# Performance work log

Hardware: AMD Instinct MI355X
Metric: run time of the kernel (lower is better)

Reference implementation:

```python
import jax, jax.numpy as jnp
import numpy as np

B, T, D = 256, 128, 1024
H = 128          # lstm_hidden
CF = 128         # conv_filters
K = 9            # num_labels
CE_W = 0.2
EPS = 1e-5


def conv1d(x, w, b, pad):
    # x: (B, C, T), w: (O, I, k)
    y = jax.lax.conv_general_dilated(x, w, (1,), [(pad, pad)],
                                     dimension_numbers=('NCH', 'OIH', 'NCH'))
    return y + b[None, :, None]


def batchnorm(x, g, beta):
    # training-mode BN over (N, W) per channel, biased variance (torch default)
    m = x.mean(axis=(0, 2), keepdims=True)
    v = x.var(axis=(0, 2), keepdims=True)
    return (x - m) * jax.lax.rsqrt(v + EPS) * g[None, :, None] + beta[None, :, None]


def lstm_dir(x, Wih, Whh, bih, bhh, reverse):
    # x: (B, T, D_in). PyTorch gate order: i, f, g, o.
    xg = jnp.einsum('btd,gd->btg', x, Wih) + bih + bhh  # (B, T, 4H)
    h0 = jnp.zeros((x.shape[0], Whh.shape[1]), x.dtype)
    c0 = jnp.zeros_like(h0)

    def step(carry, g_t):
        h, c = carry
        gates = g_t + h @ Whh.T
        i, f, g, o = jnp.split(gates, 4, axis=-1)
        c = jax.nn.sigmoid(f) * c + jax.nn.sigmoid(i) * jnp.tanh(g)
        h = jax.nn.sigmoid(o) * jnp.tanh(c)
        return (h, c), h

    _, hs = jax.lax.scan(step, (h0, c0), jnp.swapaxes(xg, 0, 1), reverse=reverse)
    return jnp.swapaxes(hs, 0, 1)  # (B, T, H)


def crf_log_partition(em, mask, start, trans, end):
    # em: (B, T, K), mask: (B, T) bool (mask[:,0] assumed True)
    score = start[None, :] + em[:, 0]  # (B, K)

    def step(score, inp):
        em_t, m_t = inp  # (B, K), (B,)
        nxt = jax.nn.logsumexp(score[:, :, None] + trans[None] + em_t[:, None, :], axis=1)
        return jnp.where(m_t[:, None], nxt, score), None

    score, _ = jax.lax.scan(step, score,
                            (jnp.swapaxes(em[:, 1:], 0, 1), jnp.swapaxes(mask[:, 1:], 0, 1)))
    return jax.nn.logsumexp(score + end[None, :], axis=1)  # (B,)


def crf_numerator(em, tags, mask, start, trans, end):
    mf = mask.astype(em.dtype)
    em_sc = jnp.take_along_axis(em, tags[..., None], axis=-1)[..., 0]  # (B, T)
    tr_sc = trans[tags[:, :-1], tags[:, 1:]]                           # (B, T-1)
    seq_ends = mask.astype(jnp.int32).sum(axis=1) - 1
    last_tags = jnp.take_along_axis(tags, seq_ends[:, None], axis=1)[:, 0]
    return (start[tags[:, 0]] + em_sc[:, 0]
            + ((tr_sc + em_sc[:, 1:]) * mf[:, 1:]).sum(axis=1)
            + end[last_tags])


def setup_inputs() -> dict:
    key = jax.random.key(0)
    ks = jax.random.split(key, 32)
    s = 0.05
    inp = {
        'embeddings': jax.random.normal(ks[0], (B, T, D), jnp.float32),
        'attention_mask': jnp.ones((B, T), jnp.int32),
        'labels': jax.random.randint(ks[1], (B, T), 0, K).astype(jnp.int64),
        'conv5_w': jax.random.normal(ks[2], (CF, D, 5)) * s,
        'conv5_b': jnp.zeros((CF,)),
        'bn1_g': jnp.ones((CF,)),
        'bn1_b': jnp.zeros((CF,)),
        'Wih_f': jax.random.normal(ks[3], (4 * H, CF)) * s,
        'Whh_f': jax.random.normal(ks[4], (4 * H, H)) * s,
        'bih_f': jnp.zeros((4 * H,)),
        'bhh_f': jnp.zeros((4 * H,)),
        'Wih_b': jax.random.normal(ks[5], (4 * H, CF)) * s,
        'Whh_b': jax.random.normal(ks[6], (4 * H, H)) * s,
        'bih_b': jnp.zeros((4 * H,)),
        'bhh_b': jnp.zeros((4 * H,)),
        'conv7_w': jax.random.normal(ks[7], (CF, 2 * H, 7)) * s,
        'conv7_b': jnp.zeros((CF,)),
        'conv9_w': jax.random.normal(ks[8], (CF, 2 * H, 9)) * s,
        'conv9_b': jnp.zeros((CF,)),
        'bn2_g': jnp.ones((2 * CF,)),
        'bn2_b': jnp.zeros((2 * CF,)),
        'cls_w': jax.random.normal(ks[9], (K, 2 * CF)) * s,
        'cls_b': jnp.zeros((K,)),
        'crf_start': jax.random.normal(ks[10], (K,)) * 0.1,
        'crf_trans': jax.random.normal(ks[11], (K, K)) * 0.1,
        'crf_end': jax.random.normal(ks[12], (K,)) * 0.1,
        'class_weights': jax.random.uniform(ks[13], (K,)) + 0.5,
    }
    return inp


def reference(embeddings, attention_mask, labels, conv5_w, conv5_b, bn1_g, bn1_b,
              Wih_f, Whh_f, bih_f, bhh_f, Wih_b, Whh_b, bih_b, bhh_b,
              conv7_w, conv7_b, conv9_w, conv9_b, bn2_g, bn2_b, cls_w, cls_b,
              crf_start, crf_trans, crf_end, class_weights):
    x = embeddings.astype(jnp.float32)
    xt = jnp.swapaxes(x, 1, 2)  # (B, D, T)
    xc = jax.nn.gelu(batchnorm(conv1d(xt, conv5_w, conv5_b, 2), bn1_g, bn1_b),
                     approximate=False)
    xl = jnp.swapaxes(xc, 1, 2)  # (B, T, CF)
    hf = lstm_dir(xl, Wih_f, Whh_f, bih_f, bhh_f, reverse=False)
    hb = lstm_dir(xl, Wih_b, Whh_b, bih_b, bhh_b, reverse=True)
    lstm_out = jnp.swapaxes(jnp.concatenate([hf, hb], axis=-1), 1, 2)  # (B, 2H, T)
    c7 = conv1d(lstm_out, conv7_w, conv7_b, 3)
    c9 = conv1d(lstm_out, conv9_w, conv9_b, 4)
    feat = jax.nn.gelu(batchnorm(jnp.concatenate([c7, c9], axis=1), bn2_g, bn2_b),
                       approximate=False)
    feat = jnp.swapaxes(feat, 1, 2)  # (B, T, 2CF); dropout p=0 -> identity
    logits = jnp.einsum('btf,kf->btk', feat, cls_w) + cls_b  # (B, T, K)

    mask = (attention_mask != 0) & (labels != -100)
    mod_labels = jnp.where(labels == -100, 0, labels).astype(jnp.int32)

    num = crf_numerator(logits, mod_labels, mask, crf_start, crf_trans, crf_end)
    logZ = crf_log_partition(logits, mask, crf_start, crf_trans, crf_end)
    crf_loss = -(num - logZ).mean()

    logp = jax.nn.log_softmax(logits, axis=-1).reshape(-1, K)
    y = labels.reshape(-1)
    valid = y != -100
    yi = jnp.where(valid, y, 0).astype(jnp.int32)
    nll = -jnp.take_along_axis(logp, yi[:, None], axis=1)[:, 0]
    w = jnp.where(valid, class_weights[yi], 0.0)
    ce_loss = (w * nll).sum() / w.sum()

    return (1.0 - CE_W) * crf_loss + CE_W * ce_loss
```

## Files before the change

kernel.cpp:

```cpp
#include <hip/hip_runtime.h>
#include <hip/hip_bf16.h>
#include <math.h>

#define BB 256
#define TT 128
#define DD 1024
#define CFF 128
#define HH 128
#define G4 512
#define NK 9

typedef __attribute__((ext_vector_type(8))) short bf16x8;
typedef __attribute__((ext_vector_type(4))) float f32x4;

__device__ __forceinline__ float bf_lo(unsigned u){ union{unsigned u; float f;} v; v.u = u << 16; return v.f; }
__device__ __forceinline__ float bf_hi(unsigned u){ union{unsigned u; float f;} v; v.u = u & 0xffff0000u; return v.f; }
__device__ __forceinline__ unsigned f2bf(float x){
    union{float f; unsigned u;} v; v.f = x;
    unsigned r = v.u + 0x7fffu + ((v.u >> 16) & 1u);
    return r >> 16;
}
__device__ __forceinline__ float fsig_fast(float x){
    return __builtin_amdgcn_rcpf(1.0f + __builtin_amdgcn_exp2f(-1.44269504f * x));
}
__device__ __forceinline__ float ftanh_fast(float x){
    return 1.0f - 2.0f * __builtin_amdgcn_rcpf(1.0f + __builtin_amdgcn_exp2f(2.88539008f * x));
}
__device__ __forceinline__ float gelu_exact(float x){
    return 0.5f*x*(1.0f + erff(x*0.70710678118654752440f));
}

__global__ __launch_bounds__(256) void prep_convw_kernel(
    const float* __restrict__ w, ushort* __restrict__ Wk, int CIN, int KS, int total)
{
    int i = blockIdx.x*256 + threadIdx.x;
    if (i >= total) return;
    int k = i % KS;
    int d = (i / KS) % CIN;
    int f = i / (KS * CIN);
    Wk[((size_t)(k*128 + f))*CIN + d] = (ushort)f2bf(w[i]);
}

__global__ __launch_bounds__(256) void prep_xg_kernel(
    const float* __restrict__ Wf, const float* __restrict__ Wb,
    const float* __restrict__ bif, const float* __restrict__ bhf,
    const float* __restrict__ bib, const float* __restrict__ bhb,
    ushort* __restrict__ Wxg, float* __restrict__ bias_xg)
{
    int i = blockIdx.x*256 + threadIdx.x;
    if (i < 65536) Wxg[i] = (ushort)f2bf(Wf[i]);
    else if (i < 131072) Wxg[i] = (ushort)f2bf(Wb[i - 65536]);
    else {
        int j = i - 131072;
        if (j < 512) bias_xg[j] = bif[j] + bhf[j];
        else if (j < 1024) bias_xg[j] = bib[j-512] + bhb[j-512];
    }
}

template<int CIN, int KS, int KSE_MAX, int SPLIT, bool IN_F32, bool OUT_BF16, bool XGT = false>
__global__ __launch_bounds__(256, 1) void conv_mfma_kernel(
    const void* __restrict__ in_v,
    const ushort* __restrict__ Wk_g,
    const float* __restrict__ bias_g,
    void* __restrict__ outA_v, void* __restrict__ outB_v,
    int OS, int co)
{
    constexpr int PAD = KS / 2;
    constexpr int ROWS = 128 + 2 * PAD;
    constexpr int NSTEP = (SPLIT == 1) ? (CIN / 64) : (CIN / 32);
    constexpr int ATOT = IN_F32 ? ROWS * 8 : ROWS * 4;
    constexpr int BTOT = KSE_MAX * 128 * 4;
    constexpr int AIT = (ATOT + 255) / 256;
    constexpr int BIT = (BTOT + 255) / 256;

    __shared__ ushort A_lds[ROWS * 32];
    __shared__ ushort B_lds[KSE_MAX * 128 * 32];

    const int tid = threadIdx.x;
    const int b   = blockIdx.x;
    const int by  = blockIdx.y;
    const int z   = blockIdx.z;
    const int dbase = (SPLIT == 1) ? z * (CIN / 2) : 0;
    const int k0    = (SPLIT == 2) ? z * KSE_MAX : 0;
    const int kse   = (SPLIT == 2) ? ((z == 0) ? KSE_MAX : (KS - KSE_MAX)) : KS;
    const ushort* __restrict__ Wk = Wk_g + (size_t)by * (size_t)(128 * CIN);
    const float* __restrict__ bias = bias_g + by * 128;

    float4 aRf[AIT];
    int4   aRb[AIT];
    int4   bR[BIT];

    auto stage_load = [&](int s) {
        const int d0 = dbase + s * 32;
        if constexpr (IN_F32) {
            const float* __restrict__ inp = (const float*)in_v;
#pragma unroll
            for (int it = 0; it < AIT; ++it) {
                int i = tid + it * 256;
                float4 v = make_float4(0.f, 0.f, 0.f, 0.f);
                if (i < ATOT) {
                    int r = i >> 3, c = i & 7;
                    int t = r - PAD;
                    if (t >= 0 && t < TT)
                        v = *reinterpret_cast<const float4*>(&inp[((size_t)b * TT + t) * CIN + d0 + c * 4]);
                }
                aRf[it] = v;
            }
        } else {
            const ushort* __restrict__ inp = (const ushort*)in_v;
#pragma unroll
            for (int it = 0; it < AIT; ++it) {
                int i = tid + it * 256;
                int4 v = make_int4(0, 0, 0, 0);
                if (i < ATOT) {
                    int r = i >> 2, c = i & 3;
                    int t = r - PAD;
                    if (t >= 0 && t < TT)
                        v = *reinterpret_cast<const int4*>(&inp[((size_t)b * TT + t) * CIN + d0 + c * 8]);
                }
                aRb[it] = v;
            }
        }
#pragma unroll
        for (int it = 0; it < BIT; ++it) {
            int i = tid + it * 256;
            int kk = i >> 9;
            int rem = i & 511;
            int f = rem >> 2, c = rem & 3;
            int4 v = make_int4(0, 0, 0, 0);
            if (kk < kse)
                v = *reinterpret_cast<const int4*>(&Wk[((size_t)((k0 + kk) * 128 + f)) * CIN + d0 + c * 8]);
            bR[it] = v;
        }
    };

    auto stage_write = [&]() {
        if constexpr (IN_F32) {
#pragma unroll
            for (int it = 0; it < AIT; ++it) {
                int i = tid + it * 256;
                if (i < ATOT) {
                    int r = i >> 3, c = i & 7;
                    float4 v = aRf[it];
                    ushort4 h;
                    h.x = (ushort)f2bf(v.x); h.y = (ushort)f2bf(v.y);
                    h.z = (ushort)f2bf(v.z); h.w = (ushort)f2bf(v.w);
                    int slot = (c >> 1) ^ (r & 3);
                    *reinterpret_cast<ushort4*>(&A_lds[r * 32 + slot * 8 + (c & 1) * 4]) = h;
                }
            }
        } else {
#pragma unroll
            for (int it = 0; it < AIT; ++it) {
                int i = tid + it * 256;
                if (i < ATOT) {
                    int r = i >> 2, c = i & 3;
                    int slot = c ^ (r & 3);
                    *reinterpret_cast<int4*>(&A_lds[r * 32 + slot * 8]) = aRb[it];
                }
            }
        }
#pragma unroll
        for (int it = 0; it < BIT; ++it) {
            int i = tid + it * 256;
            int kk = i >> 9;
            int rem = i & 511;
            int f = rem >> 2, c = rem & 3;
            int slot = c ^ (f & 3);
            *reinterpret_cast<int4*>(&B_lds[(kk * 128 + f) * 32 + slot * 8]) = bR[it];
        }
    };

    const int lane = tid & 63;
    const int wave = tid >> 6;
    const int lr = lane & 15;
    const int lk = lane >> 4;
    const int wm = wave >> 1;
    const int wn = wave & 1;

    f32x4 acc[4][4];
#pragma unroll
    for (int m = 0; m < 4; ++m)
#pragma unroll
        for (int n = 0; n < 4; ++n)
            acc[m][n] = (f32x4){0.f, 0.f, 0.f, 0.f};

    stage_load(0);
    stage_write();
    asm volatile("s_waitcnt lgkmcnt(0)" ::: "memory");
    __builtin_amdgcn_s_barrier();
    __builtin_amdgcn_sched_barrier(0);

    for (int s = 0; s < NSTEP; ++s) {
        if (s + 1 < NSTEP) stage_load(s + 1);
#pragma unroll
        for (int kk = 0; kk < KSE_MAX; ++kk) {
            bf16x8 af[4], bfr[4];
#pragma unroll
            for (int m = 0; m < 4; ++m) {
                int R = wm * 64 + m * 16 + lr + k0 + kk;
                if (kk >= kse) R = 0;
                af[m] = *reinterpret_cast<const bf16x8*>(&A_lds[R * 32 + ((lk ^ (R & 3)) * 8)]);
            }
#pragma unroll
            for (int n = 0; n < 4; ++n) {
                int Rb = kk * 128 + wn * 64 + n * 16 + lr;
                bfr[n] = *reinterpret_cast<const bf16x8*>(&B_lds[Rb * 32 + ((lk ^ (lr & 3)) * 8)]);
            }
#pragma unroll
            for (int m = 0; m < 4; ++m)
#pragma unroll
                for (int n = 0; n < 4; ++n)
                    acc[m][n] = __builtin_amdgcn_mfma_f32_16x16x32_bf16(af[m], bfr[n], acc[m][n], 0, 0, 0);
        }
        if (s + 1 < NSTEP) {
            asm volatile("s_waitcnt lgkmcnt(0)" ::: "memory");
            __builtin_amdgcn_s_barrier();
            __builtin_amdgcn_sched_barrier(0);
            stage_write();
            asm volatile("s_waitcnt lgkmcnt(0)" ::: "memory");
            __builtin_amdgcn_s_barrier();
            __builtin_amdgcn_sched_barrier(0);
        }
    }

    const bool addb = (SPLIT == 0) || (z == 0);
    void* out_v = (SPLIT != 0 && z == 1) ? outB_v : outA_v;
    float bv[4];
#pragma unroll
    for (int n = 0; n < 4; ++n) bv[n] = addb ? bias[wn * 64 + n * 16 + lr] : 0.f;
#pragma unroll
    for (int m = 0; m < 4; ++m) {
#pragma unroll
        for (int n = 0; n < 4; ++n) {
            int f = wn * 64 + n * 16 + lr;
#pragma unroll
            for (int q = 0; q < 4; ++q) {
                int trow = wm * 64 + m * 16 + lk * 4 + q;
                float val = acc[m][n][q] + bv[n];
                size_t idx;
                if constexpr (XGT) {
                    int dirg = by >> 2;
                    int g = by & 3;
                    idx = (size_t)dirg * 16777216u + (size_t)trow * 131072u
                        + (size_t)b * 512u + (size_t)(g * 128 + f);
                } else {
                    idx = ((size_t)b * TT + trow) * (size_t)OS + co + f;
                }
                if constexpr (OUT_BF16)
                    ((ushort*)out_v)[idx] = (ushort)f2bf(val);
                else
                    ((float*)out_v)[idx] = val;
            }
        }
    }
}

__global__ __launch_bounds__(256) void bn_stats_kernel(
    const float* __restrict__ y, const float* __restrict__ y2, int C, int rows_per_blk,
    float* __restrict__ sum, float* __restrict__ sqsum)
{
    int tpc = 256 / C;
    int c = threadIdx.x & (C - 1);
    int sub = threadIdx.x / C;
    size_t r0 = (size_t)blockIdx.x * rows_per_blk;
    float s = 0.f, s2 = 0.f;
    for (int r = sub; r < rows_per_blk; r += tpc) {
        size_t i = (r0 + r)*C + c;
        float v = y[i] + y2[i];
        s += v; s2 += v*v;
    }
    __shared__ float ls[256], ls2[256];
    ls[threadIdx.x] = s; ls2[threadIdx.x] = s2;
    __syncthreads();
    if (sub == 0) {
        for (int k = 1; k < tpc; ++k) { s += ls[c + k*C]; s2 += ls2[c + k*C]; }
        atomicAdd(&sum[c], s);
        atomicAdd(&sqsum[c], s2);
    }
}

__global__ __launch_bounds__(256) void bn_gelu_bf16_kernel(
    const float* __restrict__ y, const float* __restrict__ y2,
    const float* __restrict__ sum, const float* __restrict__ sqsum,
    const float* __restrict__ g, const float* __restrict__ beta,
    ushort* __restrict__ out, float inv_n)
{
    size_t i = (size_t)blockIdx.x*256 + threadIdx.x;
    int c = (int)(i & 127);
    float m = sum[c] * inv_n;
    float var = fmaxf(sqsum[c]*inv_n - m*m, 0.f);
    float xv = (y[i] + y2[i] - m) * rsqrtf(var + 1e-5f) * g[c] + beta[c];
    out[i] = (ushort)f2bf(gelu_exact(xv));
}

__global__ __launch_bounds__(512, 1) void lstm_mfma_kernel(
    const ushort* __restrict__ xg2,
    const float* __restrict__ Whhf, const float* __restrict__ Whhb,
    ushort* __restrict__ hfb)
{
    const int tid = threadIdx.x;
    const int lane = tid & 63;
    const int w = tid >> 6;
    const int jc = lane & 15;
    const int kq = lane >> 4;
    const int dir = blockIdx.x >> 4;
    const int b0 = (blockIdx.x & 15) << 4;
    const float* __restrict__ Whh = dir ? Whhb : Whhf;

    bf16x8 Wf[4][4];
#pragma unroll
    for (int g = 0; g < 4; ++g) {
        const float* wr = &Whh[(size_t)((g << 7) + (w << 4) + jc) * HH + (kq << 3)];
#pragma unroll
        for (int s = 0; s < 4; ++s) {
            float4 v0 = *reinterpret_cast<const float4*>(wr + (s << 5));
            float4 v1 = *reinterpret_cast<const float4*>(wr + (s << 5) + 4);
            union { bf16x8 v; ushort u[8]; } pk;
            pk.u[0] = (ushort)f2bf(v0.x); pk.u[1] = (ushort)f2bf(v0.y);
            pk.u[2] = (ushort)f2bf(v0.z); pk.u[3] = (ushort)f2bf(v0.w);
            pk.u[4] = (ushort)f2bf(v1.x); pk.u[5] = (ushort)f2bf(v1.y);
            pk.u[6] = (ushort)f2bf(v1.z); pk.u[7] = (ushort)f2bf(v1.w);
            Wf[g][s] = pk.v;
        }
    }

    __shared__ ushort h_lds[2][16 * 136];
    for (int i = tid; i < 16 * 136; i += 512) h_lds[0][i] = 0;
    f32x4 creg = (f32x4){0.f, 0.f, 0.f, 0.f};

    const int col0 = (w << 4) + (kq << 2);
    const int hrd = jc * 136 + (kq << 3);

    const ptrdiff_t dstep = dir ? -131072 : 131072;
    const int tt0 = dir ? (TT - 1) : 0;
    const ushort* pA = xg2 + (size_t)dir * 16777216u + (size_t)(b0 + jc) * 512u
                     + (size_t)col0 + (size_t)tt0 * 131072u;
    const ushort* pB = pA + dstep;

    uint2 xA[4], xB[4];
#pragma unroll
    for (int g = 0; g < 4; ++g) {
        xA[g] = *reinterpret_cast<const uint2*>(pA + (g << 7));
        xB[g] = *reinterpret_cast<const uint2*>(pB + (g << 7));
    }
    pA += 2 * dstep;
    pB += 2 * dstep;

    ushort* hp = hfb + (size_t)(b0 + jc) * (TT * 256) + (size_t)tt0 * 256
               + (dir << 7) + col0;
    const ptrdiff_t hstep = dir ? -256 : 256;

    __syncthreads();

    int cur = 0;

    auto step = [&](uint2 (&xr)[4], const ushort*& pp) {
        f32x4 acc[4];
#pragma unroll
        for (int g = 0; g < 4; ++g) {
            acc[g][0] = bf_lo(xr[g].x);
            acc[g][1] = bf_hi(xr[g].x);
            acc[g][2] = bf_lo(xr[g].y);
            acc[g][3] = bf_hi(xr[g].y);
        }
#pragma unroll
        for (int g = 0; g < 4; ++g)
            xr[g] = *reinterpret_cast<const uint2*>(pp + (g << 7));
        pp += 2 * dstep;
        bf16x8 Hf[4];
#pragma unroll
        for (int s = 0; s < 4; ++s)
            Hf[s] = *reinterpret_cast<const bf16x8*>(&h_lds[cur][hrd + (s << 5)]);
#pragma unroll
        for (int s = 0; s < 4; ++s)
#pragma unroll
            for (int g = 0; g < 4; ++g)
                acc[g] = __builtin_amdgcn_mfma_f32_16x16x32_bf16(Wf[g][s], Hf[s], acc[g], 0, 0, 0);
        float hv[4];
#pragma unroll
        for (int r = 0; r < 4; ++r) {
            float iv = fsig_fast(acc[0][r]);
            float fv = fsig_fast(acc[1][r]);
            float gv = ftanh_fast(acc[2][r]);
            float ov = fsig_fast(acc[3][r]);
            float c = fv * creg[r] + iv * gv;
            creg[r] = c;
            hv[r] = ov * ftanh_fast(c);
        }
        uint2 hb;
        asm("v_cvt_pk_bf16_f32 %0, %1, %2" : "=v"(hb.x) : "v"(hv[0]), "v"(hv[1]));
        asm("v_cvt_pk_bf16_f32 %0, %1, %2" : "=v"(hb.y) : "v"(hv[2]), "v"(hv[3]));
        const int nxt = cur ^ 1;
        *reinterpret_cast<uint2*>(&h_lds[nxt][jc * 136 + col0]) = hb;
        asm volatile("s_waitcnt lgkmcnt(0)" ::: "memory");
        __builtin_amdgcn_s_barrier();
        __builtin_amdgcn_sched_barrier(0);
        *reinterpret_cast<uint2*>(hp) = hb;
        hp += hstep;
        cur = nxt;
    };

    for (int t = 0; t < TT; t += 2) {
        step(xA, pA);
        step(xB, pB);
    }
}

__global__ __launch_bounds__(256) void logits_bn_kernel(
    const float* __restrict__ a, const float* __restrict__ bpart,
    const float* __restrict__ sum, const float* __restrict__ sqsum,
    const float* __restrict__ g, const float* __restrict__ beta,
    const float* __restrict__ cw, const float* __restrict__ cb,
    float* __restrict__ lg, float inv_n)
{
    __shared__ float wls[NK*256];
    __shared__ float sc_lds[256], sh_lds[256];
    for (int i = threadIdx.x; i < NK*256; i += 256) wls[i] = cw[i];
    {
        int c = threadIdx.x;
        float m = sum[c] * inv_n;
        float var = fmaxf(sqsum[c]*inv_n - m*m, 0.f);
        float rs = rsqrtf(var + 1e-5f);
        float s = rs * g[c];
        sc_lds[c] = s;
        sh_lds[c] = beta[c] - m * s;
    }
    __syncthreads();
    size_t row = (size_t)blockIdx.x*256 + threadIdx.x;
    const float* ar = &a[row*256];
    const float* br = &bpart[row*256];
    float acc[NK];
#pragma unroll
    for (int k = 0; k < NK; ++k) acc[k] = 0.f;
    for (int c = 0; c < 256; c += 4) {
        float4 av = *reinterpret_cast<const float4*>(&ar[c]);
        float4 bv = *reinterpret_cast<const float4*>(&br[c]);
        float vv[4] = {av.x + bv.x, av.y + bv.y, av.z + bv.z, av.w + bv.w};
#pragma unroll
        for (int j = 0; j < 4; ++j) {
            float xv = vv[j] * sc_lds[c + j] + sh_lds[c + j];
            float f = gelu_exact(xv);
#pragma unroll
            for (int k = 0; k < NK; ++k)
                acc[k] += f * wls[k*256 + c + j];
        }
    }
#pragma unroll
    for (int k = 0; k < NK; ++k) lg[row*NK + k] = acc[k] + cb[k];
}

__global__ __launch_bounds__(256) void ce_kernel(
    const float* __restrict__ lg, const int* __restrict__ labels,
    const float* __restrict__ cw, float* __restrict__ acc2)
{
    size_t i = (size_t)blockIdx.x*256 + threadIdx.x;
    const float* l = &lg[i*NK];
    float mx = -1e30f;
#pragma unroll
    for (int k = 0; k < NK; ++k) mx = fmaxf(mx, l[k]);
    float se = 0.f;
#pragma unroll
    for (int k = 0; k < NK; ++k) se += expf(l[k] - mx);
    float lz = mx + logf(se);
    int y = labels[i];
    bool valid = (y != -100);
    int yi = valid ? y : 0;
    float nll = lz - l[yi];
    float wv = valid ? cw[yi] : 0.f;
    __shared__ float s1[256], s2[256];
    s1[threadIdx.x] = wv*nll;
    s2[threadIdx.x] = wv;
    __syncthreads();
    for (int s = 128; s > 0; s >>= 1) {
        if (threadIdx.x < s) { s1[threadIdx.x] += s1[threadIdx.x + s]; s2[threadIdx.x] += s2[threadIdx.x + s]; }
        __syncthreads();
    }
    if (threadIdx.x == 0) { atomicAdd(&acc2[0], s1[0]); atomicAdd(&acc2[1], s2[0]); }
}

__global__ __launch_bounds__(64) void crf_kernel(
    const float* __restrict__ lg, const int* __restrict__ att,
    const int* __restrict__ labels, const float* __restrict__ startv,
    const float* __restrict__ trans, const float* __restrict__ endv,
    float* __restrict__ numo, float* __restrict__ logzo)
{
    int b = blockIdx.x;
    int lane = threadIdx.x;
    int lane_c = (lane < NK) ? lane : 0;
    const float* em = &lg[(size_t)b*TT*NK];
    float tr[NK];
#pragma unroll
    for (int i = 0; i < NK; ++i) tr[i] = trans[i*NK + lane_c];
    float score = startv[lane_c] + em[lane_c];

    for (int t = 1; t < TT; ++t) {
        int lt = labels[b*TT + t];
        bool m = (att[b*TT + t] != 0) && (lt != -100);
        float vals[NK];
#pragma unroll
        for (int i = 0; i < NK; ++i)
            vals[i] = __shfl(score, i, 64) + tr[i];
        if (m) {
            float mx = vals[0];
#pragma unroll
            for (int i = 1; i < NK; ++i) mx = fmaxf(mx, vals[i]);
            float sm = 0.f;
#pragma unroll
            for (int i = 0; i < NK; ++i) sm += expf(vals[i] - mx);
            score = mx + logf(sm) + em[t*NK + lane_c];
        }
    }
    float fin = (lane < NK) ? (score + endv[lane_c]) : -1e30f;
    float mx = -1e30f;
#pragma unroll
    for (int i = 0; i < NK; ++i) mx = fmaxf(mx, __shfl(fin, i, 64));
    float sm = 0.f;
#pragma unroll
    for (int i = 0; i < NK; ++i) sm += expf(__shfl(fin, i, 64) - mx);
    if (lane == 0) logzo[b] = mx + logf(sm);

    if (lane == 0) {
        int l0 = labels[b*TT];
        int tag0 = (l0 == -100) ? 0 : l0;
        bool m0 = (att[b*TT] != 0) && (l0 != -100);
        float num = startv[tag0] + em[tag0];
        int prev = tag0;
        int cnt = m0 ? 1 : 0;
        for (int t = 1; t < TT; ++t) {
            int lt = labels[b*TT + t];
            bool m = (att[b*TT + t] != 0) && (lt != -100);
            int tag = (lt == -100) ? 0 : lt;
            if (m) { num += trans[prev*NK + tag] + em[t*NK + tag]; cnt++; }
            prev = tag;
        }
        int le = cnt - 1; if (le < 0) le = 0; if (le >= TT) le = TT - 1;
        int ll = labels[b*TT + le];
        int ltag = (ll == -100) ? 0 : ll;
        num += endv[ltag];
        numo[b] = num;
    }
}

__global__ __launch_bounds__(256) void finalize_kernel(
    const float* __restrict__ numo, const float* __restrict__ logzo,
    const float* __restrict__ acc2, float* __restrict__ out)
{
    __shared__ float red[256];
    int tid = threadIdx.x;
    red[tid] = numo[tid] - logzo[tid];
    __syncthreads();
    for (int s = 128; s > 0; s >>= 1) {
        if (tid < s) red[tid] += red[tid + s];
        __syncthreads();
    }
    if (tid == 0) {
        float crf = -(red[0] / (float)BB);
        float ce = acc2[0] / acc2[1];
        out[0] = 0.8f*crf + 0.2f*ce;
    }
}

extern "C" void kernel_launch(void* const* d_in, const int* in_sizes, int n_in,
                              void* d_out, int out_size, void* d_ws, size_t ws_size,
                              hipStream_t stream)
{
    const float* emb   = (const float*)d_in[0];
    const int*   att   = (const int*)  d_in[1];
    const int*   lab   = (const int*)  d_in[2];
    const float* c5w   = (const float*)d_in[3];
    const float* c5b   = (const float*)d_in[4];
    const float* bn1g  = (const float*)d_in[5];
    const float* bn1b  = (const float*)d_in[6];
    const float* Wihf  = (const float*)d_in[7];
    const float* Whhf  = (const float*)d_in[8];
    const float* bihf  = (const float*)d_in[9];
    const float* bhhf  = (const float*)d_in[10];
    const float* Wihb  = (const float*)d_in[11];
    const float* Whhb  = (const float*)d_in[12];
    const float* bihb  = (const float*)d_in[13];
    const float* bhhb  = (const float*)d_in[14];
    const float* c7w   = (const float*)d_in[15];
    const float* c7b   = (const float*)d_in[16];
    const float* c9w   = (const float*)d_in[17];
    const float* c9b   = (const float*)d_in[18];
    const float* bn2g  = (const float*)d_in[19];
    const float* bn2b  = (const float*)d_in[20];
    const float* clsw  = (const float*)d_in[21];
    const float* clsb  = (const float*)d_in[22];
    const float* cstart= (const float*)d_in[23];
    const float* ctrans= (const float*)d_in[24];
    const float* cend  = (const float*)d_in[25];
    const float* cwts  = (const float*)d_in[26];
    (void)in_sizes; (void)n_in; (void)out_size; (void)ws_size;

    char* wsb = (char*)d_ws;
    size_t off = 0;
    auto alloc = [&](size_t bytes) { void* p = wsb + off; off += (bytes + 255) & ~(size_t)255; return p; };
    float*  y1      = (float*) alloc((size_t)4194304*4);
    ushort* xg      = (ushort*)alloc((size_t)2*16777216*2);
    ushort* hfb     = (ushort*)alloc((size_t)8388608*2);
    ushort* y1h     = (ushort*)alloc((size_t)4194304*2);
    float*  lg      = (float*) alloc((size_t)294912*4);
    ushort* Wk5     = (ushort*)alloc((size_t)655360*2);
    ushort* Wk7     = (ushort*)alloc((size_t)229376*2);
    ushort* Wk9     = (ushort*)alloc((size_t)294912*2);
    ushort* Wxg     = (ushort*)alloc((size_t)131072*2);
    float*  bias_xg = (float*) alloc((size_t)1024*4);
    float*  stats   = (float*) alloc((size_t)2048*4);
    float* y1b  = (float*)xg;
    float* c79a = (float*)xg;
    float* c79b = (float*)(xg + 16777216);
    float* bn1s = stats;
    float* bn1q = stats + 128;
    float* bn2s = stats + 256;
    float* bn2q = stats + 512;
    float* acc2 = stats + 768;
    float* numo = stats + 770;
    float* logzo = numo + 256;

    hipMemsetAsync(stats, 0, 770*sizeof(float), stream);

    prep_convw_kernel<<<2560, 256, 0, stream>>>(c5w, Wk5, 1024, 5, 655360);
    prep_convw_kernel<<<896,  256, 0, stream>>>(c7w, Wk7, 256, 7, 229376);
    prep_convw_kernel<<<1152, 256, 0, stream>>>(c9w, Wk9, 256, 9, 294912);
    prep_xg_kernel<<<516, 256, 0, stream>>>(Wihf, Wihb, bihf, bhhf, bihb, bhhb, Wxg, bias_xg);

    conv_mfma_kernel<1024,5,5,1,true,false><<<dim3(256,1,2), 256, 0, stream>>>(emb, Wk5, c5b, y1, y1b, 128, 0);
    bn_stats_kernel<<<256, 256, 0, stream>>>(y1, y1b, 128, 128, bn1s, bn1q);
    bn_gelu_bf16_kernel<<<16384, 256, 0, stream>>>(y1, y1b, bn1s, bn1q, bn1g, bn1b, y1h, 1.0f/32768.f);

    conv_mfma_kernel<128,1,1,0,false,true,true><<<dim3(256,8,1), 256, 0, stream>>>(y1h, Wxg, bias_xg, xg, nullptr, 512, 0);
    lstm_mfma_kernel<<<32, 512, 0, stream>>>(xg, Whhf, Whhb, hfb);

    conv_mfma_kernel<256,7,4,2,false,false><<<dim3(256,1,2), 256, 0, stream>>>(hfb, Wk7, c7b, c79a, c79b, 256, 0);
    conv_mfma_kernel<256,9,5,2,false,false><<<dim3(256,1,2), 256, 0, stream>>>(hfb, Wk9, c9b, c79a, c79b, 256, 128);
    bn_stats_kernel<<<256, 256, 0, stream>>>(c79a, c79b, 256, 128, bn2s, bn2q);

    logits_bn_kernel<<<128, 256, 0, stream>>>(c79a, c79b, bn2s, bn2q, bn2g, bn2b, clsw, clsb, lg, 1.0f/32768.f);
    ce_kernel<<<128, 256, 0, stream>>>(lg, lab, cwts, acc2);
    crf_kernel<<<BB, 64, 0, stream>>>(lg, att, lab, cstart, ctrans, cend, numo, logzo);
    finalize_kernel<<<1, 256, 0, stream>>>(numo, logzo, acc2, (float*)d_out);
}
```

Baseline: 494.2 us.

## Fuse conv7 and conv9 into one launch with zero-padded taps

Pads the 7-tap conv weights to 9 taps and stacks them with conv9 weights so one conv launch computes both via blockIdx.y channel offset. The LSTM step now computes xg addresses from the time index and stores h to global before the barrier, using software bf16 rounding instead of the packed convert instruction. The logits kernel uses smaller blocks for more parallelism. The padded taps add extra MFMA work for the conv7 half, and the software rounding adds ALU work to the recurrent critical path.

```diff
diff --git a/kernel.cpp b/kernel.cpp
--- a/kernel.cpp
+++ b/kernel.cpp
@@ -31,33 +31,41 @@
 }
 
 __global__ __launch_bounds__(256) void prep_convw_kernel(
-    const float* __restrict__ w, ushort* __restrict__ Wk, int CIN, int KS, int total)
+    const float* __restrict__ w, ushort* __restrict__ Wk,
+    int CIN, int KS_SRC, int KS_OUT, int KOFF, int total)
 {
     int i = blockIdx.x*256 + threadIdx.x;
     if (i >= total) return;
-    int k = i % KS;
-    int d = (i / KS) % CIN;
-    int f = i / (KS * CIN);
-    Wk[((size_t)(k*128 + f))*CIN + d] = (ushort)f2bf(w[i]);
+    int k = i % KS_OUT;
+    int d = (i / KS_OUT) % CIN;
+    int f = i / (KS_OUT * CIN);
+    int ks = k - KOFF;
+    float v = (ks >= 0 && ks < KS_SRC) ? w[((size_t)f*CIN + d)*KS_SRC + ks] : 0.f;
+    Wk[((size_t)(k*128 + f))*CIN + d] = (ushort)f2bf(v);
 }
 
 __global__ __launch_bounds__(256) void prep_xg_kernel(
     const float* __restrict__ Wf, const float* __restrict__ Wb,
     const float* __restrict__ bif, const float* __restrict__ bhf,
     const float* __restrict__ bib, const float* __restrict__ bhb,
-    ushort* __restrict__ Wxg, float* __restrict__ bias_xg)
+    const float* __restrict__ c7b, const float* __restrict__ c9b,
+    ushort* __restrict__ Wxg, float* __restrict__ bias_xg, float* __restrict__ cb79)
 {
     int i = blockIdx.x*256 + threadIdx.x;
     if (i < 65536) Wxg[i] = (ushort)f2bf(Wf[i]);
     else if (i < 131072) Wxg[i] = (ushort)f2bf(Wb[i - 65536]);
-    else {
+    else if (i < 132096) {
         int j = i - 131072;
         if (j < 512) bias_xg[j] = bif[j] + bhf[j];
-        else if (j < 1024) bias_xg[j] = bib[j-512] + bhb[j-512];
-    }
-}
-
-template<int CIN, int KS, int KSE_MAX, int SPLIT, bool IN_F32, bool OUT_BF16, bool XGT = false>
+        else bias_xg[j] = bib[j-512] + bhb[j-512];
+    } else if (i < 132352) {
+        int j = i - 132096;
+        cb79[j] = (j < 128) ? c7b[j] : c9b[j - 128];
+    }
+}
+
+template<int CIN, int KS, int KSE_MAX, int SPLIT, bool IN_F32, bool OUT_BF16,
+         bool XGT = false, bool CO_BY = false>
 __global__ __launch_bounds__(256, 1) void conv_mfma_kernel(
     const void* __restrict__ in_v,
     const ushort* __restrict__ Wk_g,
@@ -83,8 +91,9 @@
     const int dbase = (SPLIT == 1) ? z * (CIN / 2) : 0;
     const int k0    = (SPLIT == 2) ? z * KSE_MAX : 0;
     const int kse   = (SPLIT == 2) ? ((z == 0) ? KSE_MAX : (KS - KSE_MAX)) : KS;
-    const ushort* __restrict__ Wk = Wk_g + (size_t)by * (size_t)(128 * CIN);
+    const ushort* __restrict__ Wk = Wk_g + (size_t)by * (size_t)(128 * CIN * KS);
     const float* __restrict__ bias = bias_g + by * 128;
+    const int co_eff = co + (CO_BY ? (by << 7) : 0);
 
     float4 aRf[AIT];
     int4   aRb[AIT];
@@ -245,7 +254,7 @@
                     idx = (size_t)dirg * 16777216u + (size_t)trow * 131072u
                         + (size_t)b * 512u + (size_t)(g * 128 + f);
                 } else {
-                    idx = ((size_t)b * TT + trow) * (size_t)OS + co + f;
+                    idx = ((size_t)b * TT + trow) * (size_t)OS + co_eff + f;
                 }
                 if constexpr (OUT_BF16)
                     ((ushort*)out_v)[idx] = (ushort)f2bf(val);
@@ -329,33 +338,28 @@
     for (int i = tid; i < 16 * 136; i += 512) h_lds[0][i] = 0;
     f32x4 creg = (f32x4){0.f, 0.f, 0.f, 0.f};
 
+    const ushort* __restrict__ xb = xg2 + (size_t)dir * 16777216u
+        + (size_t)(b0 + jc) * 512u + (size_t)((w << 4) + (kq << 2));
+
+    uint2 xA[4], xB[4];
+    {
+        int tt0 = dir ? (TT - 1) : 0;
+        int tt1 = dir ? (TT - 2) : 1;
+#pragma unroll
+        for (int g = 0; g < 4; ++g) {
+            xA[g] = *reinterpret_cast<const uint2*>(xb + (size_t)tt0 * 131072u + (g << 7));
+            xB[g] = *reinterpret_cast<const uint2*>(xb + (size_t)tt1 * 131072u + (g << 7));
+        }
+    }
+
+    __syncthreads();
+
+    int cur = 0;
+    const int hrd = jc * 136 + (kq << 3);
     const int col0 = (w << 4) + (kq << 2);
-    const int hrd = jc * 136 + (kq << 3);
-
-    const ptrdiff_t dstep = dir ? -131072 : 131072;
-    const int tt0 = dir ? (TT - 1) : 0;
-    const ushort* pA = xg2 + (size_t)dir * 16777216u + (size_t)(b0 + jc) * 512u
-                     + (size_t)col0 + (size_t)tt0 * 131072u;
-    const ushort* pB = pA + dstep;
-
-    uint2 xA[4], xB[4];
-#pragma unroll
-    for (int g = 0; g < 4; ++g) {
-        xA[g] = *reinterpret_cast<const uint2*>(pA + (g << 7));
-        xB[g] = *reinterpret_cast<const uint2*>(pB + (g << 7));
-    }
-    pA += 2 * dstep;
-    pB += 2 * dstep;
-
-    ushort* hp = hfb + (size_t)(b0 + jc) * (TT * 256) + (size_t)tt0 * 256
-               + (dir << 7) + col0;
-    const ptrdiff_t hstep = dir ? -256 : 256;
-
-    __syncthreads();
-
-    int cur = 0;
-
-    auto step = [&](uint2 (&xr)[4], const ushort*& pp) {
+
+    auto step = [&](int t, uint2 (&xr)[4]) {
+        const int tt_c = dir ? (TT - 1 - t) : t;
         f32x4 acc[4];
 #pragma unroll
         for (int g = 0; g < 4; ++g) {
@@ -364,10 +368,13 @@
             acc[g][2] = bf_lo(xr[g].y);
             acc[g][3] = bf_hi(xr[g].y);
         }
-#pragma unroll
-        for (int g = 0; g < 4; ++g)
-            xr[g] = *reinterpret_cast<const uint2*>(pp + (g << 7));
-        pp += 2 * dstep;
+        {
+            int t2 = t + 2; if (t2 >= TT) t2 = TT - 1;
+            int ttn = dir ? (TT - 1 - t2) : t2;
+#pragma unroll
+            for (int g = 0; g < 4; ++g)
+                xr[g] = *reinterpret_cast<const uint2*>(xb + (size_t)ttn * 131072u + (g << 7));
+        }
         bf16x8 Hf[4];
 #pragma unroll
         for (int s = 0; s < 4; ++s)
@@ -388,26 +395,25 @@
             creg[r] = c;
             hv[r] = ov * ftanh_fast(c);
         }
-        uint2 hb;
-        asm("v_cvt_pk_bf16_f32 %0, %1, %2" : "=v"(hb.x) : "v"(hv[0]), "v"(hv[1]));
-        asm("v_cvt_pk_bf16_f32 %0, %1, %2" : "=v"(hb.y) : "v"(hv[2]), "v"(hv[3]));
+        ushort4 hb;
+        hb.x = (ushort)f2bf(hv[0]); hb.y = (ushort)f2bf(hv[1]);
+        hb.z = (ushort)f2bf(hv[2]); hb.w = (ushort)f2bf(hv[3]);
         const int nxt = cur ^ 1;
-        *reinterpret_cast<uint2*>(&h_lds[nxt][jc * 136 + col0]) = hb;
+        *reinterpret_cast<ushort4*>(&h_lds[nxt][jc * 136 + col0]) = hb;
+        *reinterpret_cast<ushort4*>(&hfb[((size_t)(b0 + jc) * TT + tt_c) * 256 + (dir << 7) + col0]) = hb;
         asm volatile("s_waitcnt lgkmcnt(0)" ::: "memory");
         __builtin_amdgcn_s_barrier();
         __builtin_amdgcn_sched_barrier(0);
-        *reinterpret_cast<uint2*>(hp) = hb;
-        hp += hstep;
         cur = nxt;
     };
 
     for (int t = 0; t < TT; t += 2) {
-        step(xA, pA);
-        step(xB, pB);
-    }
-}
-
-__global__ __launch_bounds__(256) void logits_bn_kernel(
+        step(t, xA);
+        step(t + 1, xB);
+    }
+}
+
+__global__ __launch_bounds__(128) void logits_bn_kernel(
     const float* __restrict__ a, const float* __restrict__ bpart,
     const float* __restrict__ sum, const float* __restrict__ sqsum,
     const float* __restrict__ g, const float* __restrict__ beta,
@@ -416,9 +422,8 @@
 {
     __shared__ float wls[NK*256];
     __shared__ float sc_lds[256], sh_lds[256];
-    for (int i = threadIdx.x; i < NK*256; i += 256) wls[i] = cw[i];
-    {
-        int c = threadIdx.x;
+    for (int i = threadIdx.x; i < NK*256; i += 128) wls[i] = cw[i];
+    for (int c = threadIdx.x; c < 256; c += 128) {
         float m = sum[c] * inv_n;
         float var = fmaxf(sqsum[c]*inv_n - m*m, 0.f);
         float rs = rsqrtf(var + 1e-5f);
@@ -427,7 +432,7 @@
         sh_lds[c] = beta[c] - m * s;
     }
     __syncthreads();
-    size_t row = (size_t)blockIdx.x*256 + threadIdx.x;
+    size_t row = (size_t)blockIdx.x*128 + threadIdx.x;
     const float* ar = &a[row*256];
     const float* br = &bpart[row*256];
     float acc[NK];
@@ -603,10 +608,10 @@
     ushort* y1h     = (ushort*)alloc((size_t)4194304*2);
     float*  lg      = (float*) alloc((size_t)294912*4);
     ushort* Wk5     = (ushort*)alloc((size_t)655360*2);
-    ushort* Wk7     = (ushort*)alloc((size_t)229376*2);
-    ushort* Wk9     = (ushort*)alloc((size_t)294912*2);
+    ushort* Wk79    = (ushort*)alloc((size_t)589824*2);
     ushort* Wxg     = (ushort*)alloc((size_t)131072*2);
     float*  bias_xg = (float*) alloc((size_t)1024*4);
+    float*  cb79    = (float*) alloc((size_t)256*4);
     float*  stats   = (float*) alloc((size_t)2048*4);
     float* y1b  = (float*)xg;
     float* c79a = (float*)xg;
@@ -621,10 +626,10 @@
 
     hipMemsetAsync(stats, 0, 770*sizeof(float), stream);
 
-    prep_convw_kernel<<<2560, 256, 0, stream>>>(c5w, Wk5, 1024, 5, 655360);
-    prep_convw_kernel<<<896,  256, 0, stream>>>(c7w, Wk7, 256, 7, 229376);
-    prep_convw_kernel<<<1152, 256, 0, stream>>>(c9w, Wk9, 256, 9, 294912);
-    prep_xg_kernel<<<516, 256, 0, stream>>>(Wihf, Wihb, bihf, bhhf, bihb, bhhb, Wxg, bias_xg);
+    prep_convw_kernel<<<2560, 256, 0, stream>>>(c5w, Wk5, 1024, 5, 5, 0, 655360);
+    prep_convw_kernel<<<1152, 256, 0, stream>>>(c7w, Wk79, 256, 7, 9, 1, 294912);
+    prep_convw_kernel<<<1152, 256, 0, stream>>>(c9w, Wk79 + 294912, 256, 9, 9, 0, 294912);
+    prep_xg_kernel<<<518, 256, 0, stream>>>(Wihf, Wihb, bihf, bhhf, bihb, bhhb, c7b, c9b, Wxg, bias_xg, cb79);
 
     conv_mfma_kernel<1024,5,5,1,true,false><<<dim3(256,1,2), 256, 0, stream>>>(emb, Wk5, c5b, y1, y1b, 128, 0);
     bn_stats_kernel<<<256, 256, 0, stream>>>(y1, y1b, 128, 128, bn1s, bn1q);
@@ -633,11 +638,10 @@
     conv_mfma_kernel<128,1,1,0,false,true,true><<<dim3(256,8,1), 256, 0, stream>>>(y1h, Wxg, bias_xg, xg, nullptr, 512, 0);
     lstm_mfma_kernel<<<32, 512, 0, stream>>>(xg, Whhf, Whhb, hfb);
 
-    conv_mfma_kernel<256,7,4,2,false,false><<<dim3(256,1,2), 256, 0, stream>>>(hfb, Wk7, c7b, c79a, c79b, 256, 0);
-    conv_mfma_kernel<256,9,5,2,false,false><<<dim3(256,1,2), 256, 0, stream>>>(hfb, Wk9, c9b, c79a, c79b, 256, 128);
+    conv_mfma_kernel<256,9,5,2,false,false,false,true><<<dim3(256,2,2), 256, 0, stream>>>(hfb, Wk79, cb79, c79a, c79b, 256, 0);
     bn_stats_kernel<<<256, 256, 0, stream>>>(c79a, c79b, 256, 128, bn2s, bn2q);
 
-    logits_bn_kernel<<<128, 256, 0, stream>>>(c79a, c79b, bn2s, bn2q, bn2g, bn2b, clsw, clsb, lg, 1.0f/32768.f);
+    logits_bn_kernel<<<256, 128, 0, stream>>>(c79a, c79b, bn2s, bn2q, bn2g, bn2b, clsw, clsb, lg, 1.0f/32768.f);
     ce_kernel<<<128, 256, 0, stream>>>(lg, lab, cwts, acc2);
     crf_kernel<<<BB, 64, 0, stream>>>(lg, att, lab, cstart, ctrans, cend, numo, logzo);
     finalize_kernel<<<1, 256, 0, stream>>>(numo, logzo, acc2, (float*)d_out);
```

Result: faster. 481.2 us (-2.6%).
